# Kernel optimization log

Hardware: AMD Instinct MI355X
Metric: run time of the kernel (lower is better)

## Reference

```python
import jax, jax.numpy as jnp
import numpy as np

DIM = 512
H = 8
D = DIM // H  # head_dim = 64
B, N = 2, 2048


def setup_inputs() -> dict:
    key = jax.random.key(0)
    ks = jax.random.split(key, 12)
    s = 1.0 / np.sqrt(DIM)
    inp = {
        "x": jax.random.normal(ks[0], (B, N, DIM), jnp.float32),
        "geo_bias": jax.random.normal(ks[1], (B, H, N, N), jnp.float32),
        "Wq": jax.random.normal(ks[2], (DIM, DIM), jnp.float32) * s,
        "bq": jnp.zeros((DIM,), jnp.float32),
        "Wk": jax.random.normal(ks[3], (DIM, DIM), jnp.float32) * s,
        "bk": jnp.zeros((DIM,), jnp.float32),
        "Wv": jax.random.normal(ks[4], (DIM, DIM), jnp.float32) * s,
        "bv": jnp.zeros((DIM,), jnp.float32),
        "Wo": jax.random.normal(ks[5], (DIM, DIM), jnp.float32) * s,
        "bo": jnp.zeros((DIM,), jnp.float32),
    }
    return inp


def reference(x, geo_bias, Wq, bq, Wk, bk, Wv, bv, Wo, bo):
    # x: (B, N, dim); geo_bias: (B, H, N, N)
    scale = D ** -0.5
    q = (x @ Wq.T + bq).reshape(B, N, H, D)
    k = (x @ Wk.T + bk).reshape(B, N, H, D)
    v = (x @ Wv.T + bv).reshape(B, N, H, D)
    # scores: (B, H, N, N)
    attn = jnp.einsum("bihd,bjhd->bhij", q, k) * scale + geo_bias
    attn = jax.nn.softmax(attn, axis=-1)
    out = jnp.einsum("bhij,bjhd->bihd", attn, v).reshape(B, N, DIM)
    return out @ Wo.T + bo
```

## Files before the change

kernel.cpp:

```cpp
#include <hip/hip_runtime.h>
#include <math.h>

#define SCALE 0.125f

typedef __bf16 bf16;
typedef __bf16 bf16x8 __attribute__((ext_vector_type(8)));
typedef float f32x4 __attribute__((ext_vector_type(4)));

#define WS_XB   0u
#define WS_WB   4194304u
#define WS_Q    6291456u
#define WS_K    10485760u
#define WS_VT   14680064u
#define WS_AT   18874368u

__global__ __launch_bounds__(256) void convert_kernel(
    const float* __restrict__ x, const float* __restrict__ wq,
    const float* __restrict__ wk, const float* __restrict__ wv,
    const float* __restrict__ wo, bf16* __restrict__ xb, bf16* __restrict__ wb) {
  int i = blockIdx.x * 256 + threadIdx.x;
  const float4* src; bf16* dst; int off;
  if (i < 524288) { src = (const float4*)x; dst = xb; off = i; }
  else {
    int j = i - 524288;
    int wsel = j >> 16; off = j & 65535;
    const float* wl = wsel == 0 ? wq : wsel == 1 ? wk : wsel == 2 ? wv : wo;
    src = (const float4*)wl; dst = wb + (wsel << 18);
  }
  float4 v = src[off];
  union { bf16 h[4]; uint2 u; } tmp;
  tmp.h[0] = (bf16)v.x; tmp.h[1] = (bf16)v.y;
  tmp.h[2] = (bf16)v.z; tmp.h[3] = (bf16)v.w;
  ((uint2*)dst)[off] = tmp.u;
}

__global__ __launch_bounds__(256) void qkv_gemm(
    const bf16* __restrict__ xb, const bf16* __restrict__ wb,
    const float* __restrict__ bq, const float* __restrict__ bk,
    const float* __restrict__ bv, bf16* __restrict__ qws,
    bf16* __restrict__ kws, bf16* __restrict__ vtws) {
  __shared__ bf16 Al[128 * 40];
  __shared__ bf16 Bl[128 * 40];
  int t = threadIdx.x;
  int m0 = (blockIdx.x & 31) << 7;
  int n0 = (blockIdx.x >> 5) << 7;
  int lane = t & 63, w = t >> 6;
  int quad = lane >> 4, col = lane & 15;
  int mblk = (w >> 1) * 64, nblk = (w & 1) * 64;
  f32x4 acc[4][4] = {};
  for (int k0 = 0; k0 < 512; k0 += 32) {
    __syncthreads();
    for (int pass = 0; pass < 2; ++pass) {
      int c = t + (pass << 8);
      int row = c >> 2, part = c & 3;
      *(uint4*)&Al[row * 40 + part * 8] =
          *(const uint4*)&xb[(m0 + row) * 512 + k0 + part * 8];
      *(uint4*)&Bl[row * 40 + part * 8] =
          *(const uint4*)&wb[(n0 + row) * 512 + k0 + part * 8];
    }
    __syncthreads();
    bf16x8 af[4], bfv[4];
    for (int i = 0; i < 4; i++)
      af[i] = *(const bf16x8*)&Al[(mblk + i * 16 + col) * 40 + quad * 8];
    for (int i = 0; i < 4; i++)
      bfv[i] = *(const bf16x8*)&Bl[(nblk + i * 16 + col) * 40 + quad * 8];
    for (int mi = 0; mi < 4; mi++)
      for (int ni = 0; ni < 4; ni++)
        acc[mi][ni] = __builtin_amdgcn_mfma_f32_16x16x32_bf16(
            af[mi], bfv[ni], acc[mi][ni], 0, 0, 0);
  }
  for (int mi = 0; mi < 4; mi++)
    for (int ni = 0; ni < 4; ni++) {
      int n = n0 + nblk + ni * 16 + col;
      int wid = n >> 9, feat = n & 511;
      float bias = wid == 0 ? bq[feat] : wid == 1 ? bk[feat] : bv[feat];
      int h = feat >> 6, d = feat & 63;
      int mbase = m0 + mblk + mi * 16 + quad * 4;
      int bidx = mbase >> 11, seq0 = mbase & 2047;
      if (wid == 2) {
        union { bf16 h4[4]; ushort4 u4; } pk;
        for (int r = 0; r < 4; r++) pk.h4[r] = (bf16)(acc[mi][ni][r] + bias);
        *(ushort4*)&vtws[(size_t)((((bidx << 3) + h) << 6) + d) * 2048 + seq0] = pk.u4;
      } else {
        bf16* dst = wid == 0 ? qws : kws;
        for (int r = 0; r < 4; r++)
          dst[(size_t)((((bidx << 3) + h) << 11) + seq0 + r) * 64 + d] =
              (bf16)(acc[mi][ni][r] + bias);
      }
    }
}

__global__ __launch_bounds__(256, 2) void attn_kernel(
    const bf16* __restrict__ qws, const bf16* __restrict__ kws,
    const bf16* __restrict__ vtws, const float* __restrict__ gbias,
    bf16* __restrict__ attn) {
  __shared__ bf16 Kl[2][64 * 72];
  __shared__ bf16 Vl[2][64 * 72];
  __shared__ bf16 Pl[64 * 72];
  int t = threadIdx.x, lane = t & 63, w = t >> 6;
  int quad = lane >> 4, col = lane & 15;
  int bh = blockIdx.x >> 5, qt = blockIdx.x & 31;
  int q0 = qt << 6;
  const bf16* qbase = qws + (size_t)bh * 2048 * 64;
  const bf16* kbase = kws + (size_t)bh * 2048 * 64;
  const bf16* vbase = vtws + (size_t)bh * 64 * 2048;
  const float* bb = gbias + ((size_t)bh * 2048 + q0) * 2048;

  int srow = t >> 2;
  int scol = (t & 3) << 4;

  bf16x8 aq[2];
  for (int ks = 0; ks < 2; ++ks)
    aq[ks] = *(const bf16x8*)&qbase[(q0 + w * 16 + col) * 64 + ks * 32 + quad * 8];

  f32x4 o[4] = {};
  float mrow[4], lrow[4];
  for (int r = 0; r < 4; r++) { mrow[r] = -INFINITY; lrow[r] = 0.f; }

  float bc[2][16];
  for (int r = 0; r < 4; r++)
    for (int nt = 0; nt < 4; nt++) {
      const float* brow = bb + (size_t)(w * 16 + quad * 4 + r) * 2048;
      bc[0][r * 4 + nt] = brow[nt * 16 + col];
      bc[1][r * 4 + nt] = brow[64 + nt * 16 + col];
    }

  {
    *(uint4*)&Kl[0][srow * 72 + scol]     = *(const uint4*)&kbase[srow * 64 + scol];
    *(uint4*)&Kl[0][srow * 72 + scol + 8] = *(const uint4*)&kbase[srow * 64 + scol + 8];
    *(uint4*)&Vl[0][srow * 72 + scol]     = *(const uint4*)&vbase[srow * 2048 + scol];
    *(uint4*)&Vl[0][srow * 72 + scol + 8] = *(const uint4*)&vbase[srow * 2048 + scol + 8];
  }
  __syncthreads();

  for (int kt = 0; kt < 32; kt += 2) {
#pragma unroll
    for (int u = 0; u < 2; ++u) {
      const int cur = u;
      int kt_ = kt + u;
      int snxt = (kt_ + 1) << 6;

      uint4 kra = *(const uint4*)&kbase[(snxt + srow) * 64 + scol];
      uint4 krb = *(const uint4*)&kbase[(snxt + srow) * 64 + scol + 8];
      uint4 vra = *(const uint4*)&vbase[srow * 2048 + snxt + scol];
      uint4 vrb = *(const uint4*)&vbase[srow * 2048 + snxt + scol + 8];

      f32x4 s[4];
#pragma unroll
      for (int nt = 0; nt < 4; ++nt) {
        f32x4 a = {};
#pragma unroll
        for (int ks = 0; ks < 2; ++ks) {
          bf16x8 bk_ = *(const bf16x8*)&Kl[cur][(nt * 16 + col) * 72 + ks * 32 + quad * 8];
          a = __builtin_amdgcn_mfma_f32_16x16x32_bf16(aq[ks], bk_, a, 0, 0, 0);
        }
        s[nt] = a;
      }

      float p[4][4];
#pragma unroll
      for (int r = 0; r < 4; r++) {
        float sv[4];
        float mx = -INFINITY;
#pragma unroll
        for (int nt = 0; nt < 4; nt++) {
          sv[nt] = s[nt][r] * SCALE + bc[cur][r * 4 + nt];
          mx = fmaxf(mx, sv[nt]);
        }
#pragma unroll
        for (int d = 1; d < 16; d <<= 1) mx = fmaxf(mx, __shfl_xor(mx, d));
        float mnew = fmaxf(mrow[r], mx);
        float alpha = __expf(mrow[r] - mnew);
        float sum = 0.f;
#pragma unroll
        for (int nt = 0; nt < 4; nt++) {
          float e = __expf(sv[nt] - mnew);
          p[nt][r] = e; sum += e;
        }
#pragma unroll
        for (int d = 1; d < 16; d <<= 1) sum += __shfl_xor(sum, d);
        lrow[r] = lrow[r] * alpha + sum;
        mrow[r] = mnew;
#pragma unroll
        for (int dt = 0; dt < 4; ++dt) o[dt][r] *= alpha;
      }

      if (kt_ < 30) {
        int sb = (kt_ + 2) << 6;
#pragma unroll
        for (int r = 0; r < 4; r++) {
          const float* brow = bb + (size_t)(w * 16 + quad * 4 + r) * 2048 + sb;
#pragma unroll
          for (int nt = 0; nt < 4; nt++)
            bc[cur][r * 4 + nt] = brow[nt * 16 + col];
        }
      }

#pragma unroll
      for (int nt = 0; nt < 4; nt++)
#pragma unroll
        for (int r = 0; r < 4; r++)
          Pl[(w * 16 + quad * 4 + r) * 72 + nt * 16 + col] = (bf16)p[nt][r];

#pragma unroll
      for (int ks = 0; ks < 2; ++ks) {
        bf16x8 ap = *(const bf16x8*)&Pl[(w * 16 + col) * 72 + ks * 32 + quad * 8];
#pragma unroll
        for (int dt = 0; dt < 4; ++dt) {
          bf16x8 bv_ = *(const bf16x8*)&Vl[cur][(dt * 16 + col) * 72 + ks * 32 + quad * 8];
          o[dt] = __builtin_amdgcn_mfma_f32_16x16x32_bf16(ap, bv_, o[dt], 0, 0, 0);
        }
      }

      int nb = 1 - cur;
      *(uint4*)&Kl[nb][srow * 72 + scol]     = kra;
      *(uint4*)&Kl[nb][srow * 72 + scol + 8] = krb;
      *(uint4*)&Vl[nb][srow * 72 + scol]     = vra;
      *(uint4*)&Vl[nb][srow * 72 + scol + 8] = vrb;
      __syncthreads();
    }
  }

  bf16* obase = attn + (size_t)(bh >> 3) * 2048 * 512 + (bh & 7) * 64;
  for (int r = 0; r < 4; r++) {
    float inv = 1.f / lrow[r];
    int gq = q0 + w * 16 + quad * 4 + r;
    for (int dt = 0; dt < 4; ++dt)
      obase[(size_t)gq * 512 + dt * 16 + col] = (bf16)(o[dt][r] * inv);
  }
}

__global__ __launch_bounds__(256) void out_gemm(
    const bf16* __restrict__ ab, const bf16* __restrict__ wob,
    const float* __restrict__ bo, float* __restrict__ out) {
  __shared__ bf16 Al[128 * 40];
  __shared__ bf16 Bl[128 * 40];
  int t = threadIdx.x;
  int m0 = (blockIdx.x & 31) << 7;
  int n0 = (blockIdx.x >> 5) << 7;
  int lane = t & 63, w = t >> 6;
  int quad = lane >> 4, col = lane & 15;
  int mblk = (w >> 1) * 64, nblk = (w & 1) * 64;
  f32x4 acc[4][4] = {};
  for (int k0 = 0; k0 < 512; k0 += 32) {
    __syncthreads();
    for (int pass = 0; pass < 2; ++pass) {
      int c = t + (pass << 8);
      int row = c >> 2, part = c & 3;
      *(uint4*)&Al[row * 40 + part * 8] =
          *(const uint4*)&ab[(m0 + row) * 512 + k0 + part * 8];
      *(uint4*)&Bl[row * 40 + part * 8] =
          *(const uint4*)&wob[(n0 + row) * 512 + k0 + part * 8];
    }
    __syncthreads();
    bf16x8 af[4], bfv[4];
    for (int i = 0; i < 4; i++)
      af[i] = *(const bf16x8*)&Al[(mblk + i * 16 + col) * 40 + quad * 8];
    for (int i = 0; i < 4; i++)
      bfv[i] = *(const bf16x8*)&Bl[(nblk + i * 16 + col) * 40 + quad * 8];
    for (int mi = 0; mi < 4; mi++)
      for (int ni = 0; ni < 4; ni++)
        acc[mi][ni] = __builtin_amdgcn_mfma_f32_16x16x32_bf16(
            af[mi], bfv[ni], acc[mi][ni], 0, 0, 0);
  }
  for (int mi = 0; mi < 4; mi++)
    for (int ni = 0; ni < 4; ni++)
      for (int r = 0; r < 4; r++) {
        int m = m0 + mblk + mi * 16 + quad * 4 + r;
        int n = n0 + nblk + ni * 16 + col;
        out[(size_t)m * 512 + n] = acc[mi][ni][r] + bo[n];
      }
}

extern "C" void kernel_launch(void* const* d_in, const int* in_sizes, int n_in,
                              void* d_out, int out_size, void* d_ws, size_t ws_size,
                              hipStream_t stream) {
  const float* x  = (const float*)d_in[0];
  const float* gb = (const float*)d_in[1];
  const float* Wq = (const float*)d_in[2];
  const float* bq = (const float*)d_in[3];
  const float* Wk = (const float*)d_in[4];
  const float* bk = (const float*)d_in[5];
  const float* Wv = (const float*)d_in[6];
  const float* bv = (const float*)d_in[7];
  const float* Wo = (const float*)d_in[8];
  const float* bo = (const float*)d_in[9];
  float* out = (float*)d_out;
  char* ws = (char*)d_ws;
  bf16* xb   = (bf16*)(ws + WS_XB);
  bf16* wb   = (bf16*)(ws + WS_WB);
  bf16* qws  = (bf16*)(ws + WS_Q);
  bf16* kws  = (bf16*)(ws + WS_K);
  bf16* vtws = (bf16*)(ws + WS_VT);
  bf16* at   = (bf16*)(ws + WS_AT);

  hipLaunchKernelGGL(convert_kernel, dim3(3072), dim3(256), 0, stream,
                     x, Wq, Wk, Wv, Wo, xb, wb);
  hipLaunchKernelGGL(qkv_gemm, dim3(384), dim3(256), 0, stream,
                     xb, wb, bq, bk, bv, qws, kws, vtws);
  hipLaunchKernelGGL(attn_kernel, dim3(512), dim3(256), 0, stream,
                     qws, kws, vtws, gb, at);
  hipLaunchKernelGGL(out_gemm, dim3(128), dim3(256), 0, stream,
                     at, wb + 3 * 262144, bo, out);
}
```

Baseline: 440.2 us.

## Use single-wave attention blocks loading K/V into registers; halve GEMM N-tiles

The attention kernel drops to one 64-thread wave per block covering 16 query rows, with 2048 blocks. K and V fragments are loaded straight from global memory into registers: K is double-buffered and V is loaded each step. This removes the shared-memory K/V staging and the per-tile __syncthreads. Both GEMMs switch to 128x64 tiles, doubling the grid for better CU coverage. The trade-off is that each attention wave re-reads K/V from global or L2 with no sharing across waves, which raises memory traffic and register pressure.

```diff
diff --git a/kernel.cpp b/kernel.cpp
--- a/kernel.cpp
+++ b/kernel.cpp
@@ -40,14 +40,14 @@
     const float* __restrict__ bv, bf16* __restrict__ qws,
     bf16* __restrict__ kws, bf16* __restrict__ vtws) {
   __shared__ bf16 Al[128 * 40];
-  __shared__ bf16 Bl[128 * 40];
+  __shared__ bf16 Bl[64 * 40];
   int t = threadIdx.x;
   int m0 = (blockIdx.x & 31) << 7;
-  int n0 = (blockIdx.x >> 5) << 7;
+  int n0 = (blockIdx.x >> 5) << 6;
   int lane = t & 63, w = t >> 6;
   int quad = lane >> 4, col = lane & 15;
-  int mblk = (w >> 1) * 64, nblk = (w & 1) * 64;
-  f32x4 acc[4][4] = {};
+  int mblk = (w & 1) * 64, nblk = (w >> 1) * 32;
+  f32x4 acc[4][2] = {};
   for (int k0 = 0; k0 < 512; k0 += 32) {
     __syncthreads();
     for (int pass = 0; pass < 2; ++pass) {
@@ -55,22 +55,25 @@
       int row = c >> 2, part = c & 3;
       *(uint4*)&Al[row * 40 + part * 8] =
           *(const uint4*)&xb[(m0 + row) * 512 + k0 + part * 8];
+    }
+    {
+      int row = t >> 2, part = t & 3;
       *(uint4*)&Bl[row * 40 + part * 8] =
           *(const uint4*)&wb[(n0 + row) * 512 + k0 + part * 8];
     }
     __syncthreads();
-    bf16x8 af[4], bfv[4];
+    bf16x8 af[4], bfv[2];
     for (int i = 0; i < 4; i++)
       af[i] = *(const bf16x8*)&Al[(mblk + i * 16 + col) * 40 + quad * 8];
-    for (int i = 0; i < 4; i++)
+    for (int i = 0; i < 2; i++)
       bfv[i] = *(const bf16x8*)&Bl[(nblk + i * 16 + col) * 40 + quad * 8];
     for (int mi = 0; mi < 4; mi++)
-      for (int ni = 0; ni < 4; ni++)
+      for (int ni = 0; ni < 2; ni++)
         acc[mi][ni] = __builtin_amdgcn_mfma_f32_16x16x32_bf16(
             af[mi], bfv[ni], acc[mi][ni], 0, 0, 0);
   }
   for (int mi = 0; mi < 4; mi++)
-    for (int ni = 0; ni < 4; ni++) {
+    for (int ni = 0; ni < 2; ni++) {
       int n = n0 + nblk + ni * 16 + col;
       int wid = n >> 9, feat = n & 511;
       float bias = wid == 0 ? bq[feat] : wid == 1 ? bk[feat] : bv[feat];
@@ -90,74 +93,82 @@
     }
 }
 
-__global__ __launch_bounds__(256, 2) void attn_kernel(
+__global__ __launch_bounds__(64, 2) void attn_kernel(
     const bf16* __restrict__ qws, const bf16* __restrict__ kws,
     const bf16* __restrict__ vtws, const float* __restrict__ gbias,
     bf16* __restrict__ attn) {
-  __shared__ bf16 Kl[2][64 * 72];
-  __shared__ bf16 Vl[2][64 * 72];
-  __shared__ bf16 Pl[64 * 72];
-  int t = threadIdx.x, lane = t & 63, w = t >> 6;
+  __shared__ bf16 Pl[16 * 72];
+  int lane = threadIdx.x;
   int quad = lane >> 4, col = lane & 15;
-  int bh = blockIdx.x >> 5, qt = blockIdx.x & 31;
-  int q0 = qt << 6;
+  int bid = blockIdx.x;
+  int bh = bid >> 7, qt = bid & 127;
+  int q0 = qt << 4;
   const bf16* qbase = qws + (size_t)bh * 2048 * 64;
   const bf16* kbase = kws + (size_t)bh * 2048 * 64;
   const bf16* vbase = vtws + (size_t)bh * 64 * 2048;
   const float* bb = gbias + ((size_t)bh * 2048 + q0) * 2048;
 
-  int srow = t >> 2;
-  int scol = (t & 3) << 4;
-
   bf16x8 aq[2];
+#pragma unroll
   for (int ks = 0; ks < 2; ++ks)
-    aq[ks] = *(const bf16x8*)&qbase[(q0 + w * 16 + col) * 64 + ks * 32 + quad * 8];
+    aq[ks] = *(const bf16x8*)&qbase[(q0 + col) * 64 + ks * 32 + quad * 8];
 
   f32x4 o[4] = {};
   float mrow[4], lrow[4];
+#pragma unroll
   for (int r = 0; r < 4; r++) { mrow[r] = -INFINITY; lrow[r] = 0.f; }
 
+  bf16x8 k2[2][8];
   float bc[2][16];
+#pragma unroll
+  for (int nt = 0; nt < 4; ++nt)
+#pragma unroll
+    for (int ks = 0; ks < 2; ++ks)
+      k2[0][nt * 2 + ks] =
+          *(const bf16x8*)&kbase[(nt * 16 + col) * 64 + ks * 32 + quad * 8];
+#pragma unroll
   for (int r = 0; r < 4; r++)
+#pragma unroll
     for (int nt = 0; nt < 4; nt++) {
-      const float* brow = bb + (size_t)(w * 16 + quad * 4 + r) * 2048;
+      const float* brow = bb + (size_t)(quad * 4 + r) * 2048;
       bc[0][r * 4 + nt] = brow[nt * 16 + col];
       bc[1][r * 4 + nt] = brow[64 + nt * 16 + col];
     }
 
-  {
-    *(uint4*)&Kl[0][srow * 72 + scol]     = *(const uint4*)&kbase[srow * 64 + scol];
-    *(uint4*)&Kl[0][srow * 72 + scol + 8] = *(const uint4*)&kbase[srow * 64 + scol + 8];
-    *(uint4*)&Vl[0][srow * 72 + scol]     = *(const uint4*)&vbase[srow * 2048 + scol];
-    *(uint4*)&Vl[0][srow * 72 + scol + 8] = *(const uint4*)&vbase[srow * 2048 + scol + 8];
-  }
-  __syncthreads();
-
   for (int kt = 0; kt < 32; kt += 2) {
 #pragma unroll
     for (int u = 0; u < 2; ++u) {
-      const int cur = u;
+      const int cur = u, nxt = 1 - u;
       int kt_ = kt + u;
-      int snxt = (kt_ + 1) << 6;
-
-      uint4 kra = *(const uint4*)&kbase[(snxt + srow) * 64 + scol];
-      uint4 krb = *(const uint4*)&kbase[(snxt + srow) * 64 + scol + 8];
-      uint4 vra = *(const uint4*)&vbase[srow * 2048 + snxt + scol];
-      uint4 vrb = *(const uint4*)&vbase[srow * 2048 + snxt + scol + 8];
+      int s0 = kt_ << 6;
+
+      bf16x8 vr[8];
+#pragma unroll
+      for (int ks = 0; ks < 2; ++ks)
+#pragma unroll
+        for (int dt = 0; dt < 4; ++dt)
+          vr[ks * 4 + dt] = *(const bf16x8*)&vbase[
+              (size_t)(dt * 16 + col) * 2048 + s0 + ks * 32 + quad * 8];
+
+      if (kt_ < 31) {
+        int s1 = s0 + 64;
+#pragma unroll
+        for (int nt = 0; nt < 4; ++nt)
+#pragma unroll
+          for (int ks = 0; ks < 2; ++ks)
+            k2[nxt][nt * 2 + ks] = *(const bf16x8*)&kbase[
+                (s1 + nt * 16 + col) * 64 + ks * 32 + quad * 8];
+      }
 
       f32x4 s[4];
 #pragma unroll
       for (int nt = 0; nt < 4; ++nt) {
         f32x4 a = {};
-#pragma unroll
-        for (int ks = 0; ks < 2; ++ks) {
-          bf16x8 bk_ = *(const bf16x8*)&Kl[cur][(nt * 16 + col) * 72 + ks * 32 + quad * 8];
-          a = __builtin_amdgcn_mfma_f32_16x16x32_bf16(aq[ks], bk_, a, 0, 0, 0);
-        }
+        a = __builtin_amdgcn_mfma_f32_16x16x32_bf16(aq[0], k2[cur][nt * 2], a, 0, 0, 0);
+        a = __builtin_amdgcn_mfma_f32_16x16x32_bf16(aq[1], k2[cur][nt * 2 + 1], a, 0, 0, 0);
         s[nt] = a;
       }
 
-      float p[4][4];
 #pragma unroll
       for (int r = 0; r < 4; r++) {
         float sv[4];
@@ -175,7 +186,7 @@
 #pragma unroll
         for (int nt = 0; nt < 4; nt++) {
           float e = __expf(sv[nt] - mnew);
-          p[nt][r] = e; sum += e;
+          s[nt][r] = e; sum += e;
         }
 #pragma unroll
         for (int d = 1; d < 16; d <<= 1) sum += __shfl_xor(sum, d);
@@ -189,7 +200,7 @@
         int sb = (kt_ + 2) << 6;
 #pragma unroll
         for (int r = 0; r < 4; r++) {
-          const float* brow = bb + (size_t)(w * 16 + quad * 4 + r) * 2048 + sb;
+          const float* brow = bb + (size_t)(quad * 4 + r) * 2048 + sb;
 #pragma unroll
           for (int nt = 0; nt < 4; nt++)
             bc[cur][r * 4 + nt] = brow[nt * 16 + col];
@@ -200,31 +211,24 @@
       for (int nt = 0; nt < 4; nt++)
 #pragma unroll
         for (int r = 0; r < 4; r++)
-          Pl[(w * 16 + quad * 4 + r) * 72 + nt * 16 + col] = (bf16)p[nt][r];
+          Pl[(quad * 4 + r) * 72 + nt * 16 + col] = (bf16)s[nt][r];
 
 #pragma unroll
       for (int ks = 0; ks < 2; ++ks) {
-        bf16x8 ap = *(const bf16x8*)&Pl[(w * 16 + col) * 72 + ks * 32 + quad * 8];
-#pragma unroll
-        for (int dt = 0; dt < 4; ++dt) {
-          bf16x8 bv_ = *(const bf16x8*)&Vl[cur][(dt * 16 + col) * 72 + ks * 32 + quad * 8];
-          o[dt] = __builtin_amdgcn_mfma_f32_16x16x32_bf16(ap, bv_, o[dt], 0, 0, 0);
-        }
-      }
-
-      int nb = 1 - cur;
-      *(uint4*)&Kl[nb][srow * 72 + scol]     = kra;
-      *(uint4*)&Kl[nb][srow * 72 + scol + 8] = krb;
-      *(uint4*)&Vl[nb][srow * 72 + scol]     = vra;
-      *(uint4*)&Vl[nb][srow * 72 + scol + 8] = vrb;
-      __syncthreads();
+        bf16x8 ap = *(const bf16x8*)&Pl[col * 72 + ks * 32 + quad * 8];
+#pragma unroll
+        for (int dt = 0; dt < 4; ++dt)
+          o[dt] = __builtin_amdgcn_mfma_f32_16x16x32_bf16(ap, vr[ks * 4 + dt], o[dt], 0, 0, 0);
+      }
     }
   }
 
   bf16* obase = attn + (size_t)(bh >> 3) * 2048 * 512 + (bh & 7) * 64;
+#pragma unroll
   for (int r = 0; r < 4; r++) {
     float inv = 1.f / lrow[r];
-    int gq = q0 + w * 16 + quad * 4 + r;
+    int gq = q0 + quad * 4 + r;
+#pragma unroll
     for (int dt = 0; dt < 4; ++dt)
       obase[(size_t)gq * 512 + dt * 16 + col] = (bf16)(o[dt][r] * inv);
   }
@@ -234,14 +238,14 @@
     const bf16* __restrict__ ab, const bf16* __restrict__ wob,
     const float* __restrict__ bo, float* __restrict__ out) {
   __shared__ bf16 Al[128 * 40];
-  __shared__ bf16 Bl[128 * 40];
+  __shared__ bf16 Bl[64 * 40];
   int t = threadIdx.x;
   int m0 = (blockIdx.x & 31) << 7;
-  int n0 = (blockIdx.x >> 5) << 7;
+  int n0 = (blockIdx.x >> 5) << 6;
   int lane = t & 63, w = t >> 6;
   int quad = lane >> 4, col = lane & 15;
-  int mblk = (w >> 1) * 64, nblk = (w & 1) * 64;
-  f32x4 acc[4][4] = {};
+  int mblk = (w & 1) * 64, nblk = (w >> 1) * 32;
+  f32x4 acc[4][2] = {};
   for (int k0 = 0; k0 < 512; k0 += 32) {
     __syncthreads();
     for (int pass = 0; pass < 2; ++pass) {
@@ -249,22 +253,25 @@
       int row = c >> 2, part = c & 3;
       *(uint4*)&Al[row * 40 + part * 8] =
           *(const uint4*)&ab[(m0 + row) * 512 + k0 + part * 8];
+    }
+    {
+      int row = t >> 2, part = t & 3;
       *(uint4*)&Bl[row * 40 + part * 8] =
           *(const uint4*)&wob[(n0 + row) * 512 + k0 + part * 8];
     }
     __syncthreads();
-    bf16x8 af[4], bfv[4];
+    bf16x8 af[4], bfv[2];
     for (int i = 0; i < 4; i++)
       af[i] = *(const bf16x8*)&Al[(mblk + i * 16 + col) * 40 + quad * 8];
-    for (int i = 0; i < 4; i++)
+    for (int i = 0; i < 2; i++)
       bfv[i] = *(const bf16x8*)&Bl[(nblk + i * 16 + col) * 40 + quad * 8];
     for (int mi = 0; mi < 4; mi++)
-      for (int ni = 0; ni < 4; ni++)
+      for (int ni = 0; ni < 2; ni++)
         acc[mi][ni] = __builtin_amdgcn_mfma_f32_16x16x32_bf16(
             af[mi], bfv[ni], acc[mi][ni], 0, 0, 0);
   }
   for (int mi = 0; mi < 4; mi++)
-    for (int ni = 0; ni < 4; ni++)
+    for (int ni = 0; ni < 2; ni++)
       for (int r = 0; r < 4; r++) {
         int m = m0 + mblk + mi * 16 + quad * 4 + r;
         int n = n0 + nblk + ni * 16 + col;
@@ -296,10 +303,10 @@
 
   hipLaunchKernelGGL(convert_kernel, dim3(3072), dim3(256), 0, stream,
                      x, Wq, Wk, Wv, Wo, xb, wb);
-  hipLaunchKernelGGL(qkv_gemm, dim3(384), dim3(256), 0, stream,
+  hipLaunchKernelGGL(qkv_gemm, dim3(768), dim3(256), 0, stream,
                      xb, wb, bq, bk, bv, qws, kws, vtws);
-  hipLaunchKernelGGL(attn_kernel, dim3(512), dim3(256), 0, stream,
+  hipLaunchKernelGGL(attn_kernel, dim3(2048), dim3(64), 0, stream,
                      qws, kws, vtws, gb, at);
-  hipLaunchKernelGGL(out_gemm, dim3(128), dim3(256), 0, stream,
+  hipLaunchKernelGGL(out_gemm, dim3(256), dim3(256), 0, stream,
                      at, wb + 3 * 262144, bo, out);
 }
```

New measurement: 488.0 us. +10.9%, slower.
